# Optimization experiments

Hardware: AMD Instinct MI355X
Metric: run time of the kernel (lower is better)

## Reference

```python
import jax, jax.numpy as jnp
import numpy as np

N_HEAD = 16
NEG_BIG = 1e10


def setup_inputs() -> dict:
    key = jax.random.key(0)
    ks = jax.random.split(key, 4)
    B, T, D = 2, 2048, 1024
    x = jax.random.normal(ks[0], (B, T, D), dtype=jnp.float32)
    w_attn = jax.random.normal(ks[1], (D, 3 * D), dtype=jnp.float32) * 0.02
    b_attn = jnp.zeros((3 * D,), dtype=jnp.float32)
    w_proj = jax.random.normal(ks[2], (D, D), dtype=jnp.float32) * 0.02
    b_proj = jnp.zeros((D,), dtype=jnp.float32)
    return {"x": x, "w_attn": w_attn, "b_attn": b_attn, "w_proj": w_proj, "b_proj": b_proj}


def reference(x, w_attn, b_attn, w_proj, b_proj):
    B, T, D = x.shape
    H = N_HEAD
    dh = D // H
    # fused QKV projection (Conv1d == addmm: x @ W + b)
    qkv = x @ w_attn + b_attn                      # [B, T, 3D]
    q, k, v = jnp.split(qkv, 3, axis=-1)
    # split heads -> [B, H, T, dh]
    q = q.reshape(B, T, H, dh).transpose(0, 2, 1, 3)
    k = k.reshape(B, T, H, dh).transpose(0, 2, 1, 3)
    v = v.reshape(B, T, H, dh).transpose(0, 2, 1, 3)
    # scores; repo scales by 1/sqrt(n_head) (its idiosyncrasy, kept faithfully)
    w = jnp.einsum('bhqd,bhkd->bhqk', q, k) / jnp.sqrt(jnp.float32(H))
    # causal mask via repo formula: w*b - 1e10*(1-b), b = tril ones
    b = jnp.tril(jnp.ones((T, T), dtype=w.dtype))
    w = w * b - NEG_BIG * (1.0 - b)
    w = jax.nn.softmax(w, axis=-1)
    a = jnp.einsum('bhqk,bhkd->bhqd', w, v)        # [B, H, T, dh]
    # merge heads
    a = a.transpose(0, 2, 1, 3).reshape(B, T, D)
    a = a @ w_proj + b_proj
    present = jnp.stack([k, v])                     # [2, B, H, T, dh]
    return a, present
```

## Files before the change

### kernel.cpp

```cpp
#include <hip/hip_runtime.h>
#include <hip/hip_bf16.h>

typedef __hip_bfloat16 bf16;
typedef unsigned short ush;
typedef __attribute__((ext_vector_type(8))) short bf16x8;
typedef __attribute__((ext_vector_type(4))) float f32x4;

#define BB 2
#define TT 2048
#define DD 1024
#define HH 16
#define DHH 64
#define MM (BB*TT)
#define N3 (3*DD)

__device__ __forceinline__ bf16  f2b(float x){ return __float2bfloat16(x); }
__device__ __forceinline__ ush   f2bu(float x){ bf16 h = __float2bfloat16(x); return *(ush*)&h; }

#define GLOAD_LDS(gp, lp) \
    __builtin_amdgcn_global_load_lds( \
        (const __attribute__((address_space(1))) void*)(gp), \
        (__attribute__((address_space(3))) void*)(lp), 16, 0, 0)

__global__ __launch_bounds__(256) void cvt_x(
    const float* __restrict__ src, ush* __restrict__ dst)
{
    const size_t i = ((size_t)blockIdx.x * 256 + threadIdx.x) * 8;
    float4 a = *(const float4*)&src[i];
    float4 b = *(const float4*)&src[i + 4];
    ushort4 u0; u0.x = f2bu(a.x); u0.y = f2bu(a.y); u0.z = f2bu(a.z); u0.w = f2bu(a.w);
    ushort4 u1; u1.x = f2bu(b.x); u1.y = f2bu(b.y); u1.z = f2bu(b.z); u1.w = f2bu(b.w);
    *(ushort4*)&dst[i] = u0;
    *(ushort4*)&dst[i + 4] = u1;
}

__global__ __launch_bounds__(256) void transpose_cvt(
    const float* __restrict__ src, ush* __restrict__ dst, int R, int C)
{
    __shared__ ush T[64][68];
    const int tid = threadIdx.x;
    const int c0 = blockIdx.x * 64;
    const int r0 = blockIdx.y * 64;

    #pragma unroll
    for (int it = 0; it < 4; it++) {
        int idx = it * 256 + tid;
        int i = idx >> 4, jf = idx & 15;
        float4 v = *(const float4*)&src[(size_t)(r0 + i) * C + c0 + jf * 4];
        T[jf * 4 + 0][i] = f2bu(v.x);
        T[jf * 4 + 1][i] = f2bu(v.y);
        T[jf * 4 + 2][i] = f2bu(v.z);
        T[jf * 4 + 3][i] = f2bu(v.w);
    }
    __syncthreads();
    #pragma unroll
    for (int it = 0; it < 4; it++) {
        int idx = it * 256 + tid;
        int j = idx >> 4, i4 = idx & 15;
        *(ushort4*)&dst[(size_t)(c0 + j) * R + r0 + i4 * 4] =
            *(const ushort4*)&T[j][i4 * 4];
    }
}

__global__ __launch_bounds__(256) void qkv_mfma(
    const ush* __restrict__ xbf, const ush* __restrict__ wT,
    const float* __restrict__ bias,
    bf16* __restrict__ qws, float* __restrict__ kout, float* __restrict__ vout,
    ush* __restrict__ kbf, ush* __restrict__ vtb, int write_bf)
{
    __shared__ __align__(16) ush As[128 * 32];
    __shared__ __align__(16) ush Bs[128 * 32];

    const int tid  = threadIdx.x;
    const int lane = tid & 63;
    const int w    = tid >> 6;
    const int n16  = lane & 15;
    const int quad = lane >> 4;
    const int row0 = blockIdx.y * 128;
    const int col0 = blockIdx.x * 128;
    const int wrow = (w >> 1) * 64;
    const int wcol = (w & 1) * 64;

    f32x4 acc[4][4];
    #pragma unroll
    for (int mb = 0; mb < 4; mb++)
        #pragma unroll
        for (int nb = 0; nb < 4; nb++) acc[mb][nb] = (f32x4){0.f,0.f,0.f,0.f};

    for (int kk0 = 0; kk0 < DD; kk0 += 32) {
        __syncthreads();
        #pragma unroll
        for (int it = 0; it < 2; it++) {
            int c = it * 256 + tid;
            int r = c >> 2, co = (c & 3) * 8;
            GLOAD_LDS(&xbf[(size_t)(row0 + r) * DD + kk0 + co], &As[c * 8]);
            GLOAD_LDS(&wT[(size_t)(col0 + r) * DD + kk0 + co], &Bs[c * 8]);
        }
        __syncthreads();

        bf16x8 af[4];
        #pragma unroll
        for (int mb = 0; mb < 4; mb++)
            af[mb] = *(const bf16x8*)&As[(wrow + mb * 16 + n16) * 32 + quad * 8];
        #pragma unroll
        for (int nb = 0; nb < 4; nb++) {
            bf16x8 bfr = *(const bf16x8*)&Bs[(wcol + nb * 16 + n16) * 32 + quad * 8];
            #pragma unroll
            for (int mb = 0; mb < 4; mb++)
                acc[mb][nb] = __builtin_amdgcn_mfma_f32_16x16x32_bf16(
                    af[mb], bfr, acc[mb][nb], 0, 0, 0);
        }
    }

    #pragma unroll
    for (int nb = 0; nb < 4; nb++) {
        const int gc = col0 + wcol + nb * 16 + n16;
        const float bv = bias[gc];
        const int which = gc >> 10;
        const int h = (gc & 1023) >> 6;
        const int d = gc & 63;
        #pragma unroll
        for (int mb = 0; mb < 4; mb++) {
            float vv[4];
            #pragma unroll
            for (int reg = 0; reg < 4; reg++) vv[reg] = acc[mb][nb][reg] + bv;
            const int gr0 = row0 + wrow + mb * 16 + quad * 4;
            const int b_ = gr0 >> 11, t0 = gr0 & 2047;
            const int bh = b_ * HH + h;
            const size_t tbase = ((size_t)bh * TT + t0) * DHH + d;
            if (which == 0) {
                #pragma unroll
                for (int reg = 0; reg < 4; reg++)
                    qws[tbase + (size_t)reg * DHH] = f2b(vv[reg]);
            } else if (which == 1) {
                #pragma unroll
                for (int reg = 0; reg < 4; reg++) kout[tbase + (size_t)reg * DHH] = vv[reg];
                if (write_bf) {
                    #pragma unroll
                    for (int reg = 0; reg < 4; reg++)
                        kbf[tbase + (size_t)reg * DHH] = f2bu(vv[reg]);
                }
            } else {
                #pragma unroll
                for (int reg = 0; reg < 4; reg++) vout[tbase + (size_t)reg * DHH] = vv[reg];
                if (write_bf) {
                    ushort4 u;
                    u.x = f2bu(vv[0]); u.y = f2bu(vv[1]);
                    u.z = f2bu(vv[2]); u.w = f2bu(vv[3]);
                    *(ushort4*)&vtb[((size_t)bh * DHH + d) * TT + t0] = u;
                }
            }
        }
    }
}

__global__ __launch_bounds__(256) void flash_attn_v3(
    const ush* __restrict__ qin, const ush* __restrict__ kbf,
    const ush* __restrict__ vtb, bf16* __restrict__ attn)
{
    __shared__ __align__(16) ush Ks[64][72];
    __shared__ __align__(16) ush Vt[64][72];
    __shared__ __align__(16) ush Ps[4][16][72];

    const int tid  = threadIdx.x;
    const int lane = tid & 63;
    const int w    = tid >> 6;
    const int n16  = lane & 15;
    const int quad = lane >> 4;
    const int bh = blockIdx.y;
    const int qi = (bh & 8) ? (31 - (int)blockIdx.x) : (int)blockIdx.x;
    const int q0 = qi * 64;
    const ush* Qb  = qin + (size_t)bh * TT * DHH;
    const ush* Kb  = kbf + (size_t)bh * TT * DHH;
    const ush* Vtb = vtb + (size_t)bh * DHH * TT;
    const int b_ = bh >> 4, h = bh & 15;

    const ush* Qp = Qb + (size_t)(q0 + w * 16 + n16) * DHH + quad * 8;
    const bf16x8 qa0 = *(const bf16x8*)&Qp[0];
    const bf16x8 qa1 = *(const bf16x8*)&Qp[32];

    const int r0c = tid >> 3, c8c = (tid & 7) * 8;
    const int r1c = (256 + tid) >> 3, c8c1 = ((256 + tid) & 7) * 8;

    bf16x8 kst[2], vst[2];
    {
        const ush* Kp = Kb;
        const ush* Vp = Vtb;
        kst[0] = *(const bf16x8*)&Kp[(size_t)r0c * DHH + c8c];
        kst[1] = *(const bf16x8*)&Kp[(size_t)r1c * DHH + c8c1];
        vst[0] = *(const bf16x8*)&Vp[(size_t)r0c * TT + c8c];
        vst[1] = *(const bf16x8*)&Vp[(size_t)r1c * TT + c8c1];
    }

    f32x4 o[4];
    #pragma unroll
    for (int db = 0; db < 4; db++) o[db] = (f32x4){0.f, 0.f, 0.f, 0.f};
    float lsum[4] = {0.f, 0.f, 0.f, 0.f};

    const int grow_base = q0 + w * 16 + quad * 4;
    const float SC = 0.25f * 1.4426950408889634f;

    for (int kt = 0; kt <= qi; kt++) {
        __syncthreads();
        *(bf16x8*)&Ks[r0c][c8c]  = kst[0];
        *(bf16x8*)&Ks[r1c][c8c1] = kst[1];
        *(bf16x8*)&Vt[r0c][c8c]  = vst[0];
        *(bf16x8*)&Vt[r1c][c8c1] = vst[1];
        __syncthreads();

        if (kt < qi) {
            const ush* Kp = Kb + (size_t)((kt + 1) * 64) * DHH;
            const ush* Vp = Vtb + (kt + 1) * 64;
            kst[0] = *(const bf16x8*)&Kp[(size_t)r0c * DHH + c8c];
            kst[1] = *(const bf16x8*)&Kp[(size_t)r1c * DHH + c8c1];
            vst[0] = *(const bf16x8*)&Vp[(size_t)r0c * TT + c8c];
            vst[1] = *(const bf16x8*)&Vp[(size_t)r1c * TT + c8c1];
        }

        f32x4 s[4];
        #pragma unroll
        for (int cb = 0; cb < 4; cb++) {
            bf16x8 kb0 = *(const bf16x8*)&Ks[cb * 16 + n16][quad * 8];
            bf16x8 kb1 = *(const bf16x8*)&Ks[cb * 16 + n16][32 + quad * 8];
            f32x4 acc = (f32x4){0.f, 0.f, 0.f, 0.f};
            acc = __builtin_amdgcn_mfma_f32_16x16x32_bf16(qa0, kb0, acc, 0, 0, 0);
            acc = __builtin_amdgcn_mfma_f32_16x16x32_bf16(qa1, kb1, acc, 0, 0, 0);
            s[cb] = acc;
        }

        const int gcol_base = kt * 64 + n16;
        #pragma unroll
        for (int reg = 0; reg < 4; reg++) {
            #pragma unroll
            for (int cb = 0; cb < 4; cb++) {
                float p = exp2f(s[cb][reg] * SC);
                if (gcol_base + cb * 16 > grow_base + reg) p = 0.f;
                lsum[reg] += p;
                Ps[w][quad * 4 + reg][cb * 16 + n16] = f2bu(p);
            }
        }

        bf16x8 pa0 = *(const bf16x8*)&Ps[w][n16][quad * 8];
        bf16x8 pa1 = *(const bf16x8*)&Ps[w][n16][32 + quad * 8];
        #pragma unroll
        for (int db = 0; db < 4; db++) {
            bf16x8 vb0 = *(const bf16x8*)&Vt[db * 16 + n16][quad * 8];
            bf16x8 vb1 = *(const bf16x8*)&Vt[db * 16 + n16][32 + quad * 8];
            o[db] = __builtin_amdgcn_mfma_f32_16x16x32_bf16(pa0, vb0, o[db], 0, 0, 0);
            o[db] = __builtin_amdgcn_mfma_f32_16x16x32_bf16(pa1, vb1, o[db], 0, 0, 0);
        }
    }

    #pragma unroll
    for (int reg = 0; reg < 4; reg++) {
        float ls = lsum[reg];
        #pragma unroll
        for (int off = 1; off < 16; off <<= 1)
            ls += __shfl_xor(ls, off);
        const float il = 1.0f / ls;
        const int t_ = grow_base + reg;
        bf16* outr = attn + ((size_t)(b_ * TT + t_)) * DD + h * 64 + n16;
        #pragma unroll
        for (int db = 0; db < 4; db++)
            outr[db * 16] = f2b(o[db][reg] * il);
    }
}

__global__ __launch_bounds__(256) void flash_attn_mfma(
    const bf16* __restrict__ qin, const float* __restrict__ kin,
    const float* __restrict__ vin, bf16* __restrict__ attn)
{
    __shared__ __align__(16) ush Qs[64][72];
    __shared__ __align__(16) ush Ks[64][72];
    __shared__ __align__(16) ush Vt[64][72];
    __shared__ __align__(16) ush Ps[4][16][72];

    const int tid  = threadIdx.x;
    const int lane = tid & 63;
    const int w    = tid >> 6;
    const int n16  = lane & 15;
    const int quad = lane >> 4;
    const int qi = blockIdx.x;
    const int bh = blockIdx.y;
    const int q0 = qi * 64;

    const ush*   Qp = (const ush*)qin + ((size_t)bh * TT + q0) * DHH;
    const float* Kb = kin + (size_t)bh * TT * DHH;
    const float* Vb = vin + (size_t)bh * TT * DHH;

    #pragma unroll
    for (int it = 0; it < 4; it++) {
        int idx = (it * 256 + tid) * 4;
        int r = idx >> 6, d = idx & 63;
        *(ushort4*)&Qs[r][d] = *(const ushort4*)&Qp[idx];
    }

    f32x4 o[4];
    #pragma unroll
    for (int db = 0; db < 4; db++) o[db] = (f32x4){0.f, 0.f, 0.f, 0.f};
    float m_old[4] = {-1e30f, -1e30f, -1e30f, -1e30f};
    float l_run[4] = {0.f, 0.f, 0.f, 0.f};

    for (int kt = 0; kt <= qi; kt++) {
        const float* Kp = Kb + (size_t)(kt * 64) * DHH;
        const float* Vp = Vb + (size_t)(kt * 64) * DHH;
        __syncthreads();
        #pragma unroll
        for (int it = 0; it < 4; it++) {
            int idx = (it * 256 + tid) * 4;
            int c = idx >> 6, d = idx & 63;
            float4 kv = *(const float4*)&Kp[idx];
            ushort4 kb;
            kb.x = f2bu(kv.x); kb.y = f2bu(kv.y); kb.z = f2bu(kv.z); kb.w = f2bu(kv.w);
            *(ushort4*)&Ks[c][d] = kb;
        }
        #pragma unroll
        for (int it = 0; it < 4; it++) {
            int c = tid & 63, d0 = (tid >> 6) * 4 + it * 16;
            float4 vv = *(const float4*)&Vp[c * 64 + d0];
            Vt[d0 + 0][c] = f2bu(vv.x);
            Vt[d0 + 1][c] = f2bu(vv.y);
            Vt[d0 + 2][c] = f2bu(vv.z);
            Vt[d0 + 3][c] = f2bu(vv.w);
        }
        __syncthreads();

        bf16x8 qa0 = *(const bf16x8*)&Qs[w * 16 + n16][quad * 8];
        bf16x8 qa1 = *(const bf16x8*)&Qs[w * 16 + n16][32 + quad * 8];
        f32x4 s[4];
        #pragma unroll
        for (int cb = 0; cb < 4; cb++) {
            bf16x8 kb0 = *(const bf16x8*)&Ks[cb * 16 + n16][quad * 8];
            bf16x8 kb1 = *(const bf16x8*)&Ks[cb * 16 + n16][32 + quad * 8];
            f32x4 acc = (f32x4){0.f, 0.f, 0.f, 0.f};
            acc = __builtin_amdgcn_mfma_f32_16x16x32_bf16(qa0, kb0, acc, 0, 0, 0);
            acc = __builtin_amdgcn_mfma_f32_16x16x32_bf16(qa1, kb1, acc, 0, 0, 0);
            s[cb] = acc;
        }

        const int grow_base = q0 + w * 16 + quad * 4;
        const int gcol_base = kt * 64 + n16;
        #pragma unroll
        for (int reg = 0; reg < 4; reg++) {
            float sv[4];
            float pm = -1e30f;
            #pragma unroll
            for (int cb = 0; cb < 4; cb++) {
                float v = s[cb][reg] * 0.25f;
                if (gcol_base + cb * 16 > grow_base + reg) v = -1e10f;
                sv[cb] = v;
                pm = fmaxf(pm, v);
            }
            #pragma unroll
            for (int off = 1; off < 16; off <<= 1)
                pm = fmaxf(pm, __shfl_xor(pm, off));
            float mnew = fmaxf(m_old[reg], pm);
            float alpha = __expf(m_old[reg] - mnew);
            float ps = 0.f;
            #pragma unroll
            for (int cb = 0; cb < 4; cb++) {
                float p = __expf(sv[cb] - mnew);
                Ps[w][quad * 4 + reg][cb * 16 + n16] = f2bu(p);
                ps += p;
            }
            #pragma unroll
            for (int off = 1; off < 16; off <<= 1)
                ps += __shfl_xor(ps, off);
            l_run[reg] = l_run[reg] * alpha + ps;
            m_old[reg] = mnew;
            #pragma unroll
            for (int db = 0; db < 4; db++) o[db][reg] *= alpha;
        }
        __syncthreads();

        bf16x8 pa0 = *(const bf16x8*)&Ps[w][n16][quad * 8];
        bf16x8 pa1 = *(const bf16x8*)&Ps[w][n16][32 + quad * 8];
        #pragma unroll
        for (int db = 0; db < 4; db++) {
            bf16x8 vb0 = *(const bf16x8*)&Vt[db * 16 + n16][quad * 8];
            bf16x8 vb1 = *(const bf16x8*)&Vt[db * 16 + n16][32 + quad * 8];
            o[db] = __builtin_amdgcn_mfma_f32_16x16x32_bf16(pa0, vb0, o[db], 0, 0, 0);
            o[db] = __builtin_amdgcn_mfma_f32_16x16x32_bf16(pa1, vb1, o[db], 0, 0, 0);
        }
    }

    const int b_ = bh >> 4, h = bh & 15;
    #pragma unroll
    for (int reg = 0; reg < 4; reg++) {
        const float il = 1.0f / l_run[reg];
        const int t_ = q0 + w * 16 + quad * 4 + reg;
        bf16* outr = attn + ((size_t)(b_ * TT + t_)) * DD + h * 64 + n16;
        #pragma unroll
        for (int db = 0; db < 4; db++)
            outr[db * 16] = f2b(o[db][reg] * il);
    }
}

__global__ __launch_bounds__(256) void proj_mfma(
    const ush* __restrict__ a, const ush* __restrict__ wpT,
    const float* __restrict__ bias, float* __restrict__ out)
{
    __shared__ __align__(16) ush As[128 * 32];
    __shared__ __align__(16) ush Bs[128 * 32];

    const int tid  = threadIdx.x;
    const int lane = tid & 63;
    const int w    = tid >> 6;
    const int n16  = lane & 15;
    const int quad = lane >> 4;
    const int row0 = blockIdx.y * 128;
    const int col0 = blockIdx.x * 128;
    const int wrow = (w >> 1) * 64;
    const int wcol = (w & 1) * 64;

    f32x4 acc[4][4];
    #pragma unroll
    for (int mb = 0; mb < 4; mb++)
        #pragma unroll
        for (int nb = 0; nb < 4; nb++) acc[mb][nb] = (f32x4){0.f,0.f,0.f,0.f};

    for (int kk0 = 0; kk0 < DD; kk0 += 32) {
        __syncthreads();
        #pragma unroll
        for (int it = 0; it < 2; it++) {
            int c = it * 256 + tid;
            int r = c >> 2, co = (c & 3) * 8;
            GLOAD_LDS(&a[(size_t)(row0 + r) * DD + kk0 + co], &As[c * 8]);
            GLOAD_LDS(&wpT[(size_t)(col0 + r) * DD + kk0 + co], &Bs[c * 8]);
        }
        __syncthreads();

        bf16x8 af[4];
        #pragma unroll
        for (int mb = 0; mb < 4; mb++)
            af[mb] = *(const bf16x8*)&As[(wrow + mb * 16 + n16) * 32 + quad * 8];
        #pragma unroll
        for (int nb = 0; nb < 4; nb++) {
            bf16x8 bfr = *(const bf16x8*)&Bs[(wcol + nb * 16 + n16) * 32 + quad * 8];
            #pragma unroll
            for (int mb = 0; mb < 4; mb++)
                acc[mb][nb] = __builtin_amdgcn_mfma_f32_16x16x32_bf16(
                    af[mb], bfr, acc[mb][nb], 0, 0, 0);
        }
    }

    #pragma unroll
    for (int nb = 0; nb < 4; nb++) {
        const int gc = col0 + wcol + nb * 16 + n16;
        const float bv = bias[gc];
        #pragma unroll
        for (int mb = 0; mb < 4; mb++) {
            #pragma unroll
            for (int reg = 0; reg < 4; reg++) {
                const int gr = row0 + wrow + mb * 16 + quad * 4 + reg;
                out[(size_t)gr * DD + gc] = acc[mb][nb][reg] + bv;
            }
        }
    }
}

extern "C" void kernel_launch(void* const* d_in, const int* in_sizes, int n_in,
                              void* d_out, int out_size, void* d_ws, size_t ws_size,
                              hipStream_t stream) {
    const float *x = nullptr, *w_attn = nullptr, *b_attn = nullptr,
                *w_proj = nullptr, *b_proj = nullptr;
    for (int i = 0; i < n_in; i++) {
        switch (in_sizes[i]) {
            case 4194304: x      = (const float*)d_in[i]; break;
            case 3145728: w_attn = (const float*)d_in[i]; break;
            case 3072:    b_attn = (const float*)d_in[i]; break;
            case 1048576: w_proj = (const float*)d_in[i]; break;
            case 1024:    b_proj = (const float*)d_in[i]; break;
            default: break;
        }
    }
    if (!x || !w_attn || !b_attn || !w_proj || !b_proj) return;

    float* out_a = (float*)d_out;
    float* out_k = out_a + (size_t)MM * DD;
    float* out_v = out_k + (size_t)BB * HH * TT * DHH;

    const size_t MB = 1024 * 1024;
    char* wsc = (char*)d_ws;
    ush*  wT     = (ush*)(wsc + 0);
    bf16* attnws = (bf16*)(wsc + 0);
    bf16* qws    = (bf16*)(wsc + 8 * MB);
    ush*  wpT    = (ush*)(wsc + 8 * MB);
    ush*  xbf    = (ush*)d_out;

    if (ws_size >= 32 * MB) {
        ush* kbf = (ush*)(wsc + 16 * MB);
        ush* vtb = (ush*)(wsc + 24 * MB);
        cvt_x<<<dim3(MM * DD / (256 * 8)), 256, 0, stream>>>(x, xbf);
        transpose_cvt<<<dim3(N3 / 64, DD / 64), 256, 0, stream>>>(w_attn, wT, DD, N3);
        qkv_mfma<<<dim3(N3 / 128, MM / 128), 256, 0, stream>>>(
            xbf, wT, b_attn, qws, out_k, out_v, kbf, vtb, 1);
        flash_attn_v3<<<dim3(TT / 64, BB * HH), 256, 0, stream>>>(
            (const ush*)qws, kbf, vtb, attnws);
        transpose_cvt<<<dim3(DD / 64, DD / 64), 256, 0, stream>>>(w_proj, wpT, DD, DD);
        proj_mfma<<<dim3(DD / 128, MM / 128), 256, 0, stream>>>(
            (const ush*)attnws, wpT, b_proj, out_a);
    } else if (ws_size >= 16 * MB) {
        cvt_x<<<dim3(MM * DD / (256 * 8)), 256, 0, stream>>>(x, xbf);
        transpose_cvt<<<dim3(N3 / 64, DD / 64), 256, 0, stream>>>(w_attn, wT, DD, N3);
        qkv_mfma<<<dim3(N3 / 128, MM / 128), 256, 0, stream>>>(
            xbf, wT, b_attn, qws, out_k, out_v, nullptr, nullptr, 0);
        flash_attn_mfma<<<dim3(TT / 64, BB * HH), 256, 0, stream>>>(
            qws, out_k, out_v, attnws);
        transpose_cvt<<<dim3(DD / 64, DD / 64), 256, 0, stream>>>(w_proj, wpT, DD, DD);
        proj_mfma<<<dim3(DD / 128, MM / 128), 256, 0, stream>>>(
            (const ush*)attnws, wpT, b_proj, out_a);
    }
}
```

Baseline: 204.1 us.

## Double-buffer K/V tiles and software-pipeline QK^T in flash attention

```diff
diff --git a/kernel.cpp b/kernel.cpp
--- a/kernel.cpp
+++ b/kernel.cpp
@@ -112,6 +112,8 @@
         }
     }
 
+    const float qsc = write_bf ? 0.36067376022224085f : 1.0f;
+
     #pragma unroll
     for (int nb = 0; nb < 4; nb++) {
         const int gc = col0 + wcol + nb * 16 + n16;
@@ -131,7 +133,7 @@
             if (which == 0) {
                 #pragma unroll
                 for (int reg = 0; reg < 4; reg++)
-                    qws[tbase + (size_t)reg * DHH] = f2b(vv[reg]);
+                    qws[tbase + (size_t)reg * DHH] = f2b(vv[reg] * qsc);
             } else if (which == 1) {
                 #pragma unroll
                 for (int reg = 0; reg < 4; reg++) kout[tbase + (size_t)reg * DHH] = vv[reg];
@@ -154,13 +156,15 @@
     }
 }
 
-__global__ __launch_bounds__(256) void flash_attn_v3(
+#define FP 70
+
+__global__ __launch_bounds__(256) void flash_attn_v4(
     const ush* __restrict__ qin, const ush* __restrict__ kbf,
     const ush* __restrict__ vtb, bf16* __restrict__ attn)
 {
-    __shared__ __align__(16) ush Ks[64][72];
-    __shared__ __align__(16) ush Vt[64][72];
-    __shared__ __align__(16) ush Ps[4][16][72];
+    __shared__ __align__(16) ush Ks[2][64][FP];
+    __shared__ __align__(16) ush Vt[2][64][FP];
+    __shared__ __align__(16) ush Ps[4][16][FP];
 
     const int tid  = threadIdx.x;
     const int lane = tid & 63;
@@ -183,60 +187,76 @@
     const int r1c = (256 + tid) >> 3, c8c1 = ((256 + tid) & 7) * 8;
 
     bf16x8 kst[2], vst[2];
-    {
-        const ush* Kp = Kb;
-        const ush* Vp = Vtb;
-        kst[0] = *(const bf16x8*)&Kp[(size_t)r0c * DHH + c8c];
-        kst[1] = *(const bf16x8*)&Kp[(size_t)r1c * DHH + c8c1];
-        vst[0] = *(const bf16x8*)&Vp[(size_t)r0c * TT + c8c];
-        vst[1] = *(const bf16x8*)&Vp[(size_t)r1c * TT + c8c1];
-    }
+#define LOAD_TILE(kt) do { \
+        const ush* Kp_ = Kb + (size_t)((kt) * 64) * DHH; \
+        const ush* Vp_ = Vtb + (kt) * 64; \
+        kst[0] = *(const bf16x8*)&Kp_[(size_t)r0c * DHH + c8c]; \
+        kst[1] = *(const bf16x8*)&Kp_[(size_t)r1c * DHH + c8c1]; \
+        vst[0] = *(const bf16x8*)&Vp_[(size_t)r0c * TT + c8c]; \
+        vst[1] = *(const bf16x8*)&Vp_[(size_t)r1c * TT + c8c1]; \
+    } while(0)
+#define STORE_TILE(b) do { \
+        *(bf16x8*)&Ks[b][r0c][c8c]  = kst[0]; \
+        *(bf16x8*)&Ks[b][r1c][c8c1] = kst[1]; \
+        *(bf16x8*)&Vt[b][r0c][c8c]  = vst[0]; \
+        *(bf16x8*)&Vt[b][r1c][c8c1] = vst[1]; \
+    } while(0)
+#define QKT(b, sdst) do { \
+        _Pragma("unroll") \
+        for (int cb_ = 0; cb_ < 4; cb_++) { \
+            bf16x8 kb0_ = *(const bf16x8*)&Ks[b][cb_ * 16 + n16][quad * 8]; \
+            bf16x8 kb1_ = *(const bf16x8*)&Ks[b][cb_ * 16 + n16][32 + quad * 8]; \
+            f32x4 a4_ = (f32x4){0.f, 0.f, 0.f, 0.f}; \
+            a4_ = __builtin_amdgcn_mfma_f32_16x16x32_bf16(qa0, kb0_, a4_, 0, 0, 0); \
+            a4_ = __builtin_amdgcn_mfma_f32_16x16x32_bf16(qa1, kb1_, a4_, 0, 0, 0); \
+            sdst[cb_] = a4_; \
+        } \
+    } while(0)
 
     f32x4 o[4];
     #pragma unroll
     for (int db = 0; db < 4; db++) o[db] = (f32x4){0.f, 0.f, 0.f, 0.f};
     float lsum[4] = {0.f, 0.f, 0.f, 0.f};
 
-    const int grow_base = q0 + w * 16 + quad * 4;
-    const float SC = 0.25f * 1.4426950408889634f;
+    LOAD_TILE(0);
+    STORE_TILE(0);
+    __syncthreads();
+    if (qi > 0) LOAD_TILE(1);
+    f32x4 s[4], sn[4];
+    QKT(0, s);
+    int cur = 0;
 
     for (int kt = 0; kt <= qi; kt++) {
-        __syncthreads();
-        *(bf16x8*)&Ks[r0c][c8c]  = kst[0];
-        *(bf16x8*)&Ks[r1c][c8c1] = kst[1];
-        *(bf16x8*)&Vt[r0c][c8c]  = vst[0];
-        *(bf16x8*)&Vt[r1c][c8c1] = vst[1];
-        __syncthreads();
-
-        if (kt < qi) {
-            const ush* Kp = Kb + (size_t)((kt + 1) * 64) * DHH;
-            const ush* Vp = Vtb + (kt + 1) * 64;
-            kst[0] = *(const bf16x8*)&Kp[(size_t)r0c * DHH + c8c];
-            kst[1] = *(const bf16x8*)&Kp[(size_t)r1c * DHH + c8c1];
-            vst[0] = *(const bf16x8*)&Vp[(size_t)r0c * TT + c8c];
-            vst[1] = *(const bf16x8*)&Vp[(size_t)r1c * TT + c8c1];
-        }
-
-        f32x4 s[4];
-        #pragma unroll
-        for (int cb = 0; cb < 4; cb++) {
-            bf16x8 kb0 = *(const bf16x8*)&Ks[cb * 16 + n16][quad * 8];
-            bf16x8 kb1 = *(const bf16x8*)&Ks[cb * 16 + n16][32 + quad * 8];
-            f32x4 acc = (f32x4){0.f, 0.f, 0.f, 0.f};
-            acc = __builtin_amdgcn_mfma_f32_16x16x32_bf16(qa0, kb0, acc, 0, 0, 0);
-            acc = __builtin_amdgcn_mfma_f32_16x16x32_bf16(qa1, kb1, acc, 0, 0, 0);
-            s[cb] = acc;
-        }
-
-        const int gcol_base = kt * 64 + n16;
-        #pragma unroll
-        for (int reg = 0; reg < 4; reg++) {
-            #pragma unroll
-            for (int cb = 0; cb < 4; cb++) {
-                float p = exp2f(s[cb][reg] * SC);
-                if (gcol_base + cb * 16 > grow_base + reg) p = 0.f;
-                lsum[reg] += p;
-                Ps[w][quad * 4 + reg][cb * 16 + n16] = f2bu(p);
+        const bool haveNext = (kt < qi);
+        if (haveNext) {
+            __syncthreads();
+            STORE_TILE(cur ^ 1);
+            __syncthreads();
+            if (kt + 2 <= qi) LOAD_TILE(kt + 2);
+            QKT(cur ^ 1, sn);
+        }
+
+        if (kt == qi) {
+            const int rloc = w * 16 + quad * 4;
+            #pragma unroll
+            for (int reg = 0; reg < 4; reg++) {
+                #pragma unroll
+                for (int cb = 0; cb < 4; cb++) {
+                    float p = exp2f(s[cb][reg]);
+                    if (cb * 16 + n16 > rloc + reg) p = 0.f;
+                    lsum[reg] += p;
+                    Ps[w][quad * 4 + reg][cb * 16 + n16] = f2bu(p);
+                }
+            }
+        } else {
+            #pragma unroll
+            for (int reg = 0; reg < 4; reg++) {
+                #pragma unroll
+                for (int cb = 0; cb < 4; cb++) {
+                    float p = exp2f(s[cb][reg]);
+                    lsum[reg] += p;
+                    Ps[w][quad * 4 + reg][cb * 16 + n16] = f2bu(p);
+                }
             }
         }
 
@@ -244,13 +264,20 @@
         bf16x8 pa1 = *(const bf16x8*)&Ps[w][n16][32 + quad * 8];
         #pragma unroll
         for (int db = 0; db < 4; db++) {
-            bf16x8 vb0 = *(const bf16x8*)&Vt[db * 16 + n16][quad * 8];
-            bf16x8 vb1 = *(const bf16x8*)&Vt[db * 16 + n16][32 + quad * 8];
+            bf16x8 vb0 = *(const bf16x8*)&Vt[cur][db * 16 + n16][quad * 8];
+            bf16x8 vb1 = *(const bf16x8*)&Vt[cur][db * 16 + n16][32 + quad * 8];
             o[db] = __builtin_amdgcn_mfma_f32_16x16x32_bf16(pa0, vb0, o[db], 0, 0, 0);
             o[db] = __builtin_amdgcn_mfma_f32_16x16x32_bf16(pa1, vb1, o[db], 0, 0, 0);
         }
-    }
-
+
+        if (haveNext) {
+            #pragma unroll
+            for (int c2 = 0; c2 < 4; c2++) s[c2] = sn[c2];
+            cur ^= 1;
+        }
+    }
+
+    const int grow_base = q0 + w * 16 + quad * 4;
     #pragma unroll
     for (int reg = 0; reg < 4; reg++) {
         float ls = lsum[reg];
@@ -264,6 +291,9 @@
         for (int db = 0; db < 4; db++)
             outr[db * 16] = f2b(o[db][reg] * il);
     }
+#undef LOAD_TILE
+#undef STORE_TILE
+#undef QKT
 }
 
 __global__ __launch_bounds__(256) void flash_attn_mfma(
@@ -495,7 +525,7 @@
         transpose_cvt<<<dim3(N3 / 64, DD / 64), 256, 0, stream>>>(w_attn, wT, DD, N3);
         qkv_mfma<<<dim3(N3 / 128, MM / 128), 256, 0, stream>>>(
             xbf, wT, b_attn, qws, out_k, out_v, kbf, vtb, 1);
-        flash_attn_v3<<<dim3(TT / 64, BB * HH), 256, 0, stream>>>(
+        flash_attn_v4<<<dim3(TT / 64, BB * HH), 256, 0, stream>>>(
             (const ush*)qws, kbf, vtb, attnws);
         transpose_cvt<<<dim3(DD / 64, DD / 64), 256, 0, stream>>>(w_proj, wpT, DD, DD);
         proj_mfma<<<dim3(DD / 128, MM / 128), 256, 0, stream>>>(
```

Measured after the change: 223.5 us. +9.5%, slower.
